# Kernel tuning notes

Measured on AMD Instinct MI355X. Metric: run time of the kernel, lower is better.

The kernel has to match this reference:

```python
import jax, jax.numpy as jnp
import numpy as np

DIM = 1024
MLP_RATIO = 4
EPS = 1e-6


def rmsnorm(x, w):
    return x * jax.lax.rsqrt(jnp.mean(x * x, axis=-1, keepdims=True) + EPS) * w


def film(x, cond, w, b):
    # cond: [B, D] -> scale/shift: [B, D] each, broadcast over tokens
    ss = cond @ w + b  # [B, 2D]
    scale, shift = jnp.split(ss, 2, axis=-1)
    return x * (1.0 + scale[:, None, :]) + shift[:, None, :]


def setup_inputs() -> dict:
    key = jax.random.key(0)
    ks = jax.random.split(key, 16)
    B, N, D = 4, 2048, DIM
    H = D * MLP_RATIO
    s = lambda fan_in: 1.0 / np.sqrt(fan_in)
    return {
        "x": jax.random.normal(ks[0], (B, N, D), jnp.float32),
        "cond": jax.random.normal(ks[1], (B, D), jnp.float32),
        "norm1_w": jnp.ones((D,), jnp.float32),
        "film1_w": jax.random.normal(ks[2], (D, 2 * D), jnp.float32) * s(D),
        "film1_b": jnp.zeros((2 * D,), jnp.float32),
        "q_w": jax.random.normal(ks[3], (D, D), jnp.float32) * s(D),
        "q_b": jnp.zeros((D,), jnp.float32),
        "k_w": jax.random.normal(ks[4], (D, D), jnp.float32) * s(D),
        "k_b": jnp.zeros((D,), jnp.float32),
        "v_w": jax.random.normal(ks[5], (D, D), jnp.float32) * s(D),
        "v_b": jnp.zeros((D,), jnp.float32),
        "proj_w": jax.random.normal(ks[6], (D, D), jnp.float32) * s(D),
        "proj_b": jnp.zeros((D,), jnp.float32),
        "norm2_w": jnp.ones((D,), jnp.float32),
        "film2_w": jax.random.normal(ks[7], (D, 2 * D), jnp.float32) * s(D),
        "film2_b": jnp.zeros((2 * D,), jnp.float32),
        "mlp_w1": jax.random.normal(ks[8], (D, H), jnp.float32) * s(D),
        "mlp_b1": jnp.zeros((H,), jnp.float32),
        "mlp_w2": jax.random.normal(ks[9], (H, D), jnp.float32) * s(H),
        "mlp_b2": jnp.zeros((D,), jnp.float32),
    }


def reference(x, cond, norm1_w, film1_w, film1_b, q_w, q_b, k_w, k_b, v_w, v_b,
              proj_w, proj_b, norm2_w, film2_w, film2_b, mlp_w1, mlp_b1,
              mlp_w2, mlp_b2):
    B, N, D = x.shape
    x_in = x
    h = film(rmsnorm(x, norm1_w), cond, film1_w, film1_b)
    Q = h @ q_w + q_b
    K = h @ k_w + k_b
    V = h @ v_w + v_b
    scores = jnp.einsum('bnd,bmd->bnm', Q, K) * (D ** -0.5)  # [B,N,N]
    attn = jax.nn.softmax(scores, axis=-1)
    out = jnp.einsum('bnm,bmd->bnd', attn, V)
    x = x_in + (out @ proj_w + proj_b)
    x_in = x
    h = film(rmsnorm(x, norm2_w), cond, film2_w, film2_b)
    h = jax.nn.gelu(h @ mlp_w1 + mlp_b1, approximate=False) @ mlp_w2 + mlp_b2
    return x_in + h
```

## Files before the change

kernel.cpp:

```cpp
#include <hip/hip_runtime.h>
#include <math.h>

typedef unsigned short u16;
typedef __bf16 bf16;
typedef bf16 bf16x8 __attribute__((ext_vector_type(8)));
typedef float f32x4 __attribute__((ext_vector_type(4)));

#define DEV __device__ __forceinline__
#define MFMA(a, b, c) __builtin_amdgcn_mfma_f32_16x16x32_bf16(a, b, c, 0, 0, 0)

DEV u16 f2b(float f) {
  unsigned u = __builtin_bit_cast(unsigned, f);
  u += 0x7fffu + ((u >> 16) & 1u);
  return (u16)(u >> 16);
}
DEV float b2f(u16 h) {
  unsigned u = ((unsigned)h) << 16;
  return __builtin_bit_cast(float, u);
}
DEV float gelu_f(float x) {
  float e = __expf(x * (-1.5957691216f - 0.07135481283f * x * x));
  return x / (1.0f + e);
}

DEV void gl2lds16(const void* g, void* l) {
  __builtin_amdgcn_global_load_lds(
      (const __attribute__((address_space(1))) unsigned int*)g,
      (__attribute__((address_space(3))) unsigned int*)l, 16, 0, 0);
}

struct TDesc { const float* src; u16* dst; int R, C, t0, tx; };
struct T6 { TDesc d[6]; };

__global__ void k_transpose6(T6 td) {
  __shared__ float tile[32][33];
  const int id = blockIdx.x;
  TDesc d = td.d[0];
#pragma unroll
  for (int k = 1; k < 6; ++k)
    if (id >= td.d[k].t0) d = td.d[k];
  const int local = id - d.t0;
  const int c0 = (local % d.tx) * 32, r0 = (local / d.tx) * 32;
  const int tx = threadIdx.x, ty = threadIdx.y;
#pragma unroll
  for (int i = 0; i < 32; i += 8)
    tile[ty + i][tx] = d.src[(long)(r0 + ty + i) * d.C + c0 + tx];
  __syncthreads();
#pragma unroll
  for (int i = 0; i < 32; i += 8)
    d.dst[(long)(c0 + ty + i) * d.R + r0 + tx] = f2b(tile[tx][ty + i]);
}

__global__ __launch_bounds__(256) void k_film_part(const float* __restrict__ cond,
                                                   const float* __restrict__ f1w,
                                                   const float* __restrict__ f2w,
                                                   float* __restrict__ part) {
  const int j = blockIdx.x * 256 + threadIdx.x;
  const int b = blockIdx.y;
  const int z = blockIdx.z;
  const int kz = z & 7;
  const float* fw = (z < 8) ? f1w : f2w;
  const float* cp = cond + b * 1024 + kz * 128;
  const float* wp = fw + (long)kz * 128 * 2048 + j;
  float acc = 0.0f;
#pragma unroll 4
  for (int d = 0; d < 128; ++d) acc = fmaf(cp[d], wp[(long)d * 2048], acc);
  part[((z * 4 + b) << 11) + j] = acc;
}
__global__ __launch_bounds__(256) void k_film_comb(const float* __restrict__ part,
                                                   const float* __restrict__ f1b,
                                                   const float* __restrict__ f2b_,
                                                   float* __restrict__ ss) {
  const int j = blockIdx.x * 256 + threadIdx.x;
  const int b = blockIdx.y & 3, f = blockIdx.y >> 2;
  float a = (f ? f2b_ : f1b)[j];
#pragma unroll
  for (int kz = 0; kz < 8; ++kz) a += part[(((f * 8 + kz) * 4 + b) << 11) + j];
  ss[((f * 4 + b) << 11) + j] = a;
}

template <typename InT>
__global__ __launch_bounds__(256) void k_rmsfilm(const InT* __restrict__ x,
                                                 const float* __restrict__ nw,
                                                 const float* __restrict__ ss,
                                                 u16* __restrict__ h) {
  const int row = blockIdx.x;
  const int b = row >> 11;
  const int t = threadIdx.x;
  float4 v;
  if constexpr (sizeof(InT) == 4) {
    v = ((const float4*)(x + (long)row * 1024))[t];
  } else {
    ushort4 u = ((const ushort4*)(x + (long)row * 1024))[t];
    v = make_float4(b2f(u.x), b2f(u.y), b2f(u.z), b2f(u.w));
  }
  float s = v.x * v.x + v.y * v.y + v.z * v.z + v.w * v.w;
#pragma unroll
  for (int off = 32; off; off >>= 1) s += __shfl_xor(s, off);
  __shared__ float red[4];
  const int wv = t >> 6, lane = t & 63;
  if (lane == 0) red[wv] = s;
  __syncthreads();
  const float tot = red[0] + red[1] + red[2] + red[3];
  const float rn = rsqrtf(tot * (1.0f / 1024.0f) + 1e-6f);
  const float4 w4 = ((const float4*)nw)[t];
  const float4 sc = ((const float4*)(ss + b * 2048))[t];
  const float4 sh = ((const float4*)(ss + b * 2048 + 1024))[t];
  ushort4 o;
  o.x = f2b(v.x * rn * w4.x * (1.0f + sc.x) + sh.x);
  o.y = f2b(v.y * rn * w4.y * (1.0f + sc.y) + sh.y);
  o.z = f2b(v.z * rn * w4.z * (1.0f + sc.z) + sh.z);
  o.w = f2b(v.w * rn * w4.w * (1.0f + sc.w) + sh.w);
  ((ushort4*)(h + (long)row * 1024))[t] = o;
}

__global__ __launch_bounds__(256) void k_rowsuminv(const float* __restrict__ part,
                                                   float* __restrict__ inv) {
  const int id = blockIdx.x * 256 + threadIdx.x;
  float s = 0.0f;
#pragma unroll
  for (int b = 0; b < 16; ++b) s += part[b * 8192 + id];
  inv[id] = 1.0f / s;
}

enum { EB = 1, ES = 2, EG = 4, ER = 8, EQKV = 16, ERB = 32, EEXP = 64, EPVN = 128 };

template <int BN, int EPI, typename OutT>
__global__ __launch_bounds__(256, 4) void k_gemm(
    const u16* __restrict__ A, const u16* __restrict__ B, OutT* __restrict__ C,
    const float* __restrict__ bias, const float* __restrict__ bias2,
    const float* __restrict__ bias3, const float* __restrict__ resid,
    u16* __restrict__ Vt, float* __restrict__ rsum, float scale,
    int N, int K, long sAb, long sBb, long sCb) {
  constexpr int NR = BN / 32;
  constexpr int NBC = BN * 8 / 256;
  __shared__ u16 As[128 * 64];
  __shared__ u16 Bs[BN * 64];
  const int tid = threadIdx.x, lane = tid & 63, wv = tid >> 6;
  const int wr = wv >> 1, wc = wv & 1;
  const int r = lane & 15, q = lane >> 4;

  int flat = blockIdx.y * gridDim.x + blockIdx.x;
  const int nxy = gridDim.x * gridDim.y;
  flat = (flat & 7) * (nxy >> 3) + (flat >> 3);
  const int bx = flat % gridDim.x, by = flat / gridDim.x;

  const long bm = (long)by * 128, bn = (long)bx * BN;
  const u16* Ab = A + (long)blockIdx.z * sAb + bm * K;
  const u16* Bb = B + (long)blockIdx.z * sBb + bn * K;

  f32x4 acc[4][NR] = {};

  for (int k0 = 0; k0 < K; k0 += 64) {
#pragma unroll
    for (int i = 0; i < 4; ++i) {
      const int c = i * 256 + tid;
      const int row = c >> 3, sp = c & 7;
      const long g = (long)row * K + k0 + ((sp ^ (row & 7)) << 3);
      gl2lds16(Ab + g, As + c * 8);
    }
#pragma unroll
    for (int i = 0; i < NBC; ++i) {
      const int c = i * 256 + tid;
      const int row = c >> 3, sp = c & 7;
      const long g = (long)row * K + k0 + ((sp ^ (row & 7)) << 3);
      gl2lds16(Bb + g, Bs + c * 8);
    }
    __syncthreads();
    bf16x8 a[8], b[2 * NR];
#pragma unroll
    for (int kh = 0; kh < 2; ++kh) {
#pragma unroll
      for (int i = 0; i < 4; ++i) {
        const int ar = wr * 64 + i * 16 + r;
        a[kh * 4 + i] = *(const bf16x8*)&As[ar * 64 + ((kh * 4 + q) ^ (ar & 7)) * 8];
      }
#pragma unroll
      for (int ni = 0; ni < NR; ++ni) {
        const int br = wc * (BN / 2) + ni * 16 + r;
        b[kh * NR + ni] = *(const bf16x8*)&Bs[br * 64 + ((kh * 4 + q) ^ (br & 7)) * 8];
      }
    }
#pragma unroll
    for (int kh = 0; kh < 2; ++kh)
#pragma unroll
      for (int mi = 0; mi < 4; ++mi)
#pragma unroll
        for (int ni = 0; ni < NR; ++ni)
          acc[mi][ni] = MFMA(a[kh * 4 + mi], b[kh * NR + ni], acc[mi][ni]);
    __syncthreads();
  }

  const long cb = (long)blockIdx.z * sCb;
  float rs[4][4] = {};
#pragma unroll
  for (int ni = 0; ni < NR; ++ni) {
    const long col = bn + wc * (BN / 2) + ni * 16 + r;
    float bv = 0.0f;
    int reg = 0, c = (int)col;
    if constexpr ((EPI & EB) != 0) bv = bias[col];
    if constexpr ((EPI & EQKV) != 0) {
      reg = (int)(col >> 10);
      c = (int)col & 1023;
      bv = (reg == 0) ? bias[c] : (reg == 1) ? bias2[c] : bias3[c];
    }
#pragma unroll
    for (int mi = 0; mi < 4; ++mi) {
#pragma unroll
      for (int j = 0; j < 4; ++j) {
        const long row = bm + wr * 64 + mi * 16 + q * 4 + j;
        float v = acc[mi][ni][j];
        if constexpr ((EPI & ES) != 0) v *= scale;
        if constexpr ((EPI & EEXP) != 0) {
          v = __expf(v * scale);
          rs[mi][j] += v;
        }
        if constexpr ((EPI & EPVN) != 0) v *= bias[(long)blockIdx.z * 2048 + row];
        if constexpr ((EPI & (EB | EQKV)) != 0) v += bv;
        if constexpr ((EPI & EG) != 0) v = gelu_f(v);
        if constexpr ((EPI & ER) != 0) v += resid[row * N + col];
        if constexpr ((EPI & ERB) != 0) v += b2f(((const u16*)resid)[row * N + col]);
        if constexpr ((EPI & EQKV) != 0) {
          if (reg < 2)
            ((u16*)C)[(long)reg * 8388608 + row * 1024 + c] = f2b(v);
          else
            Vt[((row >> 11) << 21) + ((long)c << 11) + (row & 2047)] = f2b(v);
        } else if constexpr (sizeof(OutT) == 4) {
          C[cb + row * N + col] = v;
        } else {
          C[cb + row * N + col] = f2b(v);
        }
      }
    }
  }
  if constexpr ((EPI & EEXP) != 0) {
    float* rbuf = (float*)As;
#pragma unroll
    for (int mi = 0; mi < 4; ++mi)
#pragma unroll
      for (int j = 0; j < 4; ++j) {
        float v = rs[mi][j];
        v += __shfl_xor(v, 1);
        v += __shfl_xor(v, 2);
        v += __shfl_xor(v, 4);
        v += __shfl_xor(v, 8);
        rs[mi][j] = v;
      }
    if (r == 0) {
#pragma unroll
      for (int mi = 0; mi < 4; ++mi)
#pragma unroll
        for (int j = 0; j < 4; ++j)
          rbuf[wc * 128 + wr * 64 + mi * 16 + q * 4 + j] = rs[mi][j];
    }
    __syncthreads();
    if (tid < 128) {
      const float s = rbuf[tid] + rbuf[128 + tid];
      rsum[(long)bx * 8192 + (long)blockIdx.z * 2048 + bm + tid] = s;
    }
  }
}

extern "C" void kernel_launch(void* const* d_in, const int* in_sizes, int n_in,
                              void* d_out, int out_size, void* d_ws, size_t ws_size,
                              hipStream_t stream) {
  const float* x    = (const float*)d_in[0];
  const float* cond = (const float*)d_in[1];
  const float* n1w  = (const float*)d_in[2];
  const float* f1w  = (const float*)d_in[3];
  const float* f1b  = (const float*)d_in[4];
  const float* qw   = (const float*)d_in[5];
  const float* qb   = (const float*)d_in[6];
  const float* kw   = (const float*)d_in[7];
  const float* kb   = (const float*)d_in[8];
  const float* vw   = (const float*)d_in[9];
  const float* vb   = (const float*)d_in[10];
  const float* pw   = (const float*)d_in[11];
  const float* pb   = (const float*)d_in[12];
  const float* n2w  = (const float*)d_in[13];
  const float* f2w  = (const float*)d_in[14];
  const float* f2b_ = (const float*)d_in[15];
  const float* w1   = (const float*)d_in[16];
  const float* b1   = (const float*)d_in[17];
  const float* w2   = (const float*)d_in[18];
  const float* b2   = (const float*)d_in[19];
  float* out = (float*)d_out;

  char* ws = (char*)d_ws;
  size_t o = 0;
  auto alloc = [&](size_t bytes) {
    size_t ret = o;
    o += (bytes + 255) & ~(size_t)255;
    return ret;
  };
  const long N = 2048, D = 1024, H = 4096;

  u16* qkvT = (u16*)(ws + alloc(3 * D * D * 2));
  u16* pT   = (u16*)(ws + alloc(D * D * 2));
  u16* w1T  = (u16*)(ws + alloc(D * H * 2));
  u16* w2T  = (u16*)(ws + alloc(D * H * 2));
  float* ss    = (float*)(ws + alloc(2 * 4 * 2 * D * 4));
  float* part  = (float*)(ws + alloc(16 * 4 * 2 * D * 4));
  float* spart = (float*)(ws + alloc(16 * 8192 * 4));
  float* rsinv = (float*)(ws + alloc(8192 * 4));
  u16* h    = (u16*)(ws + alloc(4 * N * D * 2));
  u16* x1b  = (u16*)(ws + alloc(4 * N * D * 2));
  u16* AO   = (u16*)(ws + alloc(4 * N * D * 2));
  const size_t big = o;
  u16* Q    = (u16*)(ws + alloc(4 * N * D * 2));
  u16* Kb   = (u16*)(ws + alloc(4 * N * D * 2));
  u16* Vt   = (u16*)(ws + alloc(4 * N * D * 2));
  u16* S    = (u16*)(ws + alloc(4 * N * N * 2));
  u16* h1   = (u16*)(ws + big);
  (void)ws_size; (void)in_sizes; (void)n_in; (void)out_size; (void)Kb;

  T6 td;
  td.d[0] = {qw, qkvT,                1024, 1024,    0,  32};
  td.d[1] = {kw, qkvT + 1024 * 1024,  1024, 1024, 1024,  32};
  td.d[2] = {vw, qkvT + 2048 * 1024,  1024, 1024, 2048,  32};
  td.d[3] = {pw, pT,                  1024, 1024, 3072,  32};
  td.d[4] = {w1, w1T,                 1024, 4096, 4096, 128};
  td.d[5] = {w2, w2T,                 4096, 1024, 8192,  32};
  k_transpose6<<<12288, dim3(32, 8), 0, stream>>>(td);

  k_film_part<<<dim3(8, 4, 16), 256, 0, stream>>>(cond, f1w, f2w, part);
  k_film_comb<<<dim3(8, 8), 256, 0, stream>>>(part, f1b, f2b_, ss);

  k_rmsfilm<float><<<8192, 256, 0, stream>>>(x, n1w, ss, h);

  k_gemm<128, EQKV, u16><<<dim3(24, 64, 1), 256, 0, stream>>>(
      h, qkvT, Q, qb, kb, vb, nullptr, Vt, nullptr, 1.0f, 3072, 1024, 0, 0, 0);

  k_gemm<128, EEXP, u16><<<dim3(16, 16, 4), 256, 0, stream>>>(
      Q, Kb, S, nullptr, nullptr, nullptr, nullptr, nullptr, spart, 0.03125f,
      2048, 1024, N * D, N * D, N * N);
  k_rowsuminv<<<32, 256, 0, stream>>>(spart, rsinv);

  k_gemm<64, EPVN, u16><<<dim3(16, 16, 4), 256, 0, stream>>>(
      S, Vt, AO, rsinv, nullptr, nullptr, nullptr, nullptr, nullptr, 1.0f,
      1024, 2048, N * N, D * N, N * D);

  k_gemm<64, EB | ER, u16><<<dim3(16, 64, 1), 256, 0, stream>>>(
      AO, pT, x1b, pb, nullptr, nullptr, x, nullptr, nullptr, 1.0f, 1024, 1024, 0, 0, 0);

  k_rmsfilm<u16><<<8192, 256, 0, stream>>>(x1b, n2w, ss + 4 * 2048, h);

  k_gemm<128, EB | EG, u16><<<dim3(32, 64, 1), 256, 0, stream>>>(
      h, w1T, h1, b1, nullptr, nullptr, nullptr, nullptr, nullptr, 1.0f, 4096, 1024, 0, 0, 0);

  k_gemm<64, EB | ERB, float><<<dim3(16, 64, 1), 256, 0, stream>>>(
      h1, w2T, out, b2, nullptr, nullptr, (const float*)x1b, nullptr, nullptr, 1.0f,
      1024, 4096, 0, 0, 0);
}
```

Measured before the change: 394.1 us.

## Add 256x256 double-buffered 8-wave GEMM kernel for QKV, QK^T and MLP1

```diff
diff --git a/kernel.cpp b/kernel.cpp
--- a/kernel.cpp
+++ b/kernel.cpp
@@ -8,6 +8,7 @@
 
 #define DEV __device__ __forceinline__
 #define MFMA(a, b, c) __builtin_amdgcn_mfma_f32_16x16x32_bf16(a, b, c, 0, 0, 0)
+#define FENCE() asm volatile("" ::: "memory")
 
 DEV u16 f2b(float f) {
   unsigned u = __builtin_bit_cast(unsigned, f);
@@ -119,11 +120,186 @@
   const int id = blockIdx.x * 256 + threadIdx.x;
   float s = 0.0f;
 #pragma unroll
-  for (int b = 0; b < 16; ++b) s += part[b * 8192 + id];
+  for (int b = 0; b < 8; ++b) s += part[b * 8192 + id];
   inv[id] = 1.0f / s;
 }
 
 enum { EB = 1, ES = 2, EG = 4, ER = 8, EQKV = 16, ERB = 32, EEXP = 64, EPVN = 128 };
+
+template <int EPI, typename OutT>
+__global__ __launch_bounds__(512, 2) void k_gemm8(
+    const u16* __restrict__ A, const u16* __restrict__ B, OutT* __restrict__ C,
+    const float* __restrict__ bias, const float* __restrict__ bias2,
+    const float* __restrict__ bias3, u16* __restrict__ Vt,
+    float* __restrict__ rsum, float scale, int N, int K,
+    long sAb, long sBb, long sCb) {
+  __shared__ u16 sm[65536];
+  const int tid = threadIdx.x, lane = tid & 63, wid = tid >> 6;
+  const int wm = wid >> 2, wn = wid & 3;
+  const int r = lane & 15, q = lane >> 4;
+
+  int flat = blockIdx.y * gridDim.x + blockIdx.x;
+  const int nxy = gridDim.x * gridDim.y;
+  flat = (flat & 7) * (nxy >> 3) + (flat >> 3);
+  const int bx = flat % gridDim.x, by = flat / gridDim.x;
+
+  const long bm = (long)by * 256, bn = (long)bx * 256;
+  const u16* Ab = A + (long)blockIdx.z * sAb + bm * K;
+  const u16* Bb = B + (long)blockIdx.z * sBb + bn * K;
+  const int NT = K >> 6;
+
+#define STG(buf, ab, half, t)                                                   \
+  {                                                                             \
+    const u16* _s = (ab) ? Bb : Ab;                                             \
+    u16* _d = &sm[(buf) * 32768 + (ab) * 16384 + (half) * 8192];                \
+    _Pragma("unroll") for (int _i = 0; _i < 2; ++_i) {                          \
+      const int _c = _i * 512 + tid;                                            \
+      const int _row = _c >> 3, _sp = _c & 7;                                   \
+      gl2lds16(_s + (long)((half) * 128 + _row) * K + (long)(t) * 64 +          \
+                   ((_sp ^ (_row & 7)) << 3),                                   \
+               _d + _c * 8);                                                    \
+    }                                                                           \
+  }
+#define LDAq(dst, buf, qm)                                                      \
+  _Pragma("unroll") for (int _p = 0; _p < 4; ++_p)                              \
+  _Pragma("unroll") for (int _kk = 0; _kk < 2; ++_kk) {                         \
+    const int _ar = wm * 128 + (qm) * 64 + _p * 16 + r;                         \
+    dst[_p * 2 + _kk] = *(const bf16x8*)&sm[(buf) * 32768 +                     \
+        (_ar >> 7) * 8192 + (_ar & 127) * 64 + (((_kk * 4 + q) ^ (_ar & 7)) << 3)]; \
+  }
+#define LDBq(dst, buf, qn)                                                      \
+  _Pragma("unroll") for (int _p = 0; _p < 2; ++_p)                              \
+  _Pragma("unroll") for (int _kk = 0; _kk < 2; ++_kk) {                         \
+    const int _br = wn * 64 + (qn) * 32 + _p * 16 + r;                          \
+    dst[_p * 2 + _kk] = *(const bf16x8*)&sm[(buf) * 32768 + 16384 +             \
+        (_br >> 7) * 8192 + (_br & 127) * 64 + (((_kk * 4 + q) ^ (_br & 7)) << 3)]; \
+  }
+#define BAR() { FENCE(); __builtin_amdgcn_s_barrier(); FENCE(); }
+#define WAITMM() { asm volatile("s_waitcnt lgkmcnt(0)" ::: "memory"); \
+                   __builtin_amdgcn_sched_barrier(0); }
+#define VMW4() asm volatile("s_waitcnt vmcnt(4)" ::: "memory")
+#define VMW0() asm volatile("s_waitcnt vmcnt(0)" ::: "memory")
+#define MM(aa, bb, qm, qn)                                                      \
+  { __builtin_amdgcn_s_setprio(1);                                              \
+    _Pragma("unroll") for (int _p = 0; _p < 4; ++_p)                            \
+    _Pragma("unroll") for (int _n = 0; _n < 2; ++_n)                            \
+    _Pragma("unroll") for (int _kk = 0; _kk < 2; ++_kk)                         \
+      acc[(qm) * 4 + _p][(qn) * 2 + _n] =                                       \
+          MFMA(aa[_p * 2 + _kk], bb[_n * 2 + _kk], acc[(qm) * 4 + _p][(qn) * 2 + _n]); \
+    __builtin_amdgcn_s_setprio(0); }
+
+  f32x4 acc[8][4] = {};
+  STG(0, 1, 0, 0); STG(0, 1, 1, 0); STG(0, 0, 0, 0); STG(0, 0, 1, 0);
+  STG(1, 1, 0, 1); STG(1, 1, 1, 1);
+  VMW4();
+  BAR();
+
+  for (int i = 0; i < (NT >> 1); ++i) {
+    const int T = 2 * i;
+    const bool more = (T + 2) < NT;
+    bf16x8 a[8], b0[4], b1[4];
+    LDAq(a, 0, 0); LDBq(b0, 0, 0);
+    STG(1, 0, 0, T + 1);
+    BAR(); WAITMM(); MM(a, b0, 0, 0); BAR();
+    LDBq(b1, 0, 1);
+    STG(1, 0, 1, T + 1);
+    BAR(); WAITMM(); MM(a, b1, 0, 1); BAR();
+    LDAq(a, 0, 1);
+    if (more) STG(0, 1, 0, T + 2);
+    BAR(); WAITMM(); MM(a, b1, 1, 1); BAR();
+    if (more) { STG(0, 1, 1, T + 2); VMW4(); }
+    else VMW0();
+    BAR(); WAITMM(); MM(a, b0, 1, 0); BAR();
+    LDAq(a, 1, 0); LDBq(b0, 1, 0);
+    if (more) STG(0, 0, 0, T + 2);
+    BAR(); WAITMM(); MM(a, b0, 0, 0); BAR();
+    LDBq(b1, 1, 1);
+    if (more) STG(0, 0, 1, T + 2);
+    BAR(); WAITMM(); MM(a, b1, 0, 1); BAR();
+    LDAq(a, 1, 1);
+    if (more) STG(1, 1, 0, T + 3);
+    BAR(); WAITMM(); MM(a, b1, 1, 1); BAR();
+    if (more) { STG(1, 1, 1, T + 3); VMW4(); }
+    else VMW0();
+    BAR(); WAITMM(); MM(a, b0, 1, 0); BAR();
+  }
+
+  const long cb = (long)blockIdx.z * sCb;
+  float rs[8][4];
+  if constexpr ((EPI & EEXP) != 0) {
+#pragma unroll
+    for (int mi = 0; mi < 8; ++mi)
+#pragma unroll
+      for (int j = 0; j < 4; ++j) rs[mi][j] = 0.0f;
+  }
+#pragma unroll
+  for (int ni = 0; ni < 4; ++ni) {
+    const long col = bn + wn * 64 + ni * 16 + r;
+    float bv = 0.0f;
+    int reg = 0, c = (int)col;
+    if constexpr ((EPI & EB) != 0) bv = bias[col];
+    if constexpr ((EPI & EQKV) != 0) {
+      reg = (int)(col >> 10);
+      c = (int)col & 1023;
+      bv = (reg == 0) ? bias[c] : (reg == 1) ? bias2[c] : bias3[c];
+    }
+#pragma unroll
+    for (int mi = 0; mi < 8; ++mi) {
+#pragma unroll
+      for (int j = 0; j < 4; ++j) {
+        const long row = bm + wm * 128 + mi * 16 + q * 4 + j;
+        float v = acc[mi][ni][j];
+        if constexpr ((EPI & EEXP) != 0) { v = __expf(v * scale); rs[mi][j] += v; }
+        if constexpr ((EPI & (EB | EQKV)) != 0) v += bv;
+        if constexpr ((EPI & EG) != 0) v = gelu_f(v);
+        if constexpr ((EPI & EQKV) != 0) {
+          if (reg < 2)
+            ((u16*)C)[(long)reg * 8388608 + row * 1024 + c] = f2b(v);
+          else
+            Vt[((row >> 11) << 21) + ((long)c << 11) + (row & 2047)] = f2b(v);
+        } else if constexpr (sizeof(OutT) == 4) {
+          C[cb + row * N + col] = v;
+        } else {
+          C[cb + row * N + col] = f2b(v);
+        }
+      }
+    }
+  }
+  if constexpr ((EPI & EEXP) != 0) {
+    float* rbuf = (float*)sm;
+    __syncthreads();
+#pragma unroll
+    for (int mi = 0; mi < 8; ++mi)
+#pragma unroll
+      for (int j = 0; j < 4; ++j) {
+        float v = rs[mi][j];
+        v += __shfl_xor(v, 1);
+        v += __shfl_xor(v, 2);
+        v += __shfl_xor(v, 4);
+        v += __shfl_xor(v, 8);
+        rs[mi][j] = v;
+      }
+    if (r == 0) {
+#pragma unroll
+      for (int mi = 0; mi < 8; ++mi)
+#pragma unroll
+        for (int j = 0; j < 4; ++j)
+          rbuf[wn * 256 + wm * 128 + mi * 16 + q * 4 + j] = rs[mi][j];
+    }
+    __syncthreads();
+    if (tid < 256)
+      rsum[(long)bx * 8192 + (long)blockIdx.z * 2048 + bm + tid] =
+          rbuf[tid] + rbuf[256 + tid] + rbuf[512 + tid] + rbuf[768 + tid];
+  }
+#undef STG
+#undef LDAq
+#undef LDBq
+#undef BAR
+#undef WAITMM
+#undef VMW4
+#undef VMW0
+#undef MM
+}
 
 template <int BN, int EPI, typename OutT>
 __global__ __launch_bounds__(256, 4) void k_gemm(
@@ -144,6 +320,7 @@
   const int nxy = gridDim.x * gridDim.y;
   flat = (flat & 7) * (nxy >> 3) + (flat >> 3);
   const int bx = flat % gridDim.x, by = flat / gridDim.x;
+  (void)bx;
 
   const long bm = (long)by * 128, bn = (long)bx * BN;
   const u16* Ab = A + (long)blockIdx.z * sAb + bm * K;
@@ -192,18 +369,11 @@
   }
 
   const long cb = (long)blockIdx.z * sCb;
-  float rs[4][4] = {};
 #pragma unroll
   for (int ni = 0; ni < NR; ++ni) {
     const long col = bn + wc * (BN / 2) + ni * 16 + r;
     float bv = 0.0f;
-    int reg = 0, c = (int)col;
     if constexpr ((EPI & EB) != 0) bv = bias[col];
-    if constexpr ((EPI & EQKV) != 0) {
-      reg = (int)(col >> 10);
-      c = (int)col & 1023;
-      bv = (reg == 0) ? bias[c] : (reg == 1) ? bias2[c] : bias3[c];
-    }
 #pragma unroll
     for (int mi = 0; mi < 4; ++mi) {
 #pragma unroll
@@ -211,21 +381,12 @@
         const long row = bm + wr * 64 + mi * 16 + q * 4 + j;
         float v = acc[mi][ni][j];
         if constexpr ((EPI & ES) != 0) v *= scale;
-        if constexpr ((EPI & EEXP) != 0) {
-          v = __expf(v * scale);
-          rs[mi][j] += v;
-        }
         if constexpr ((EPI & EPVN) != 0) v *= bias[(long)blockIdx.z * 2048 + row];
-        if constexpr ((EPI & (EB | EQKV)) != 0) v += bv;
+        if constexpr ((EPI & EB) != 0) v += bv;
         if constexpr ((EPI & EG) != 0) v = gelu_f(v);
         if constexpr ((EPI & ER) != 0) v += resid[row * N + col];
         if constexpr ((EPI & ERB) != 0) v += b2f(((const u16*)resid)[row * N + col]);
-        if constexpr ((EPI & EQKV) != 0) {
-          if (reg < 2)
-            ((u16*)C)[(long)reg * 8388608 + row * 1024 + c] = f2b(v);
-          else
-            Vt[((row >> 11) << 21) + ((long)c << 11) + (row & 2047)] = f2b(v);
-        } else if constexpr (sizeof(OutT) == 4) {
+        if constexpr (sizeof(OutT) == 4) {
           C[cb + row * N + col] = v;
         } else {
           C[cb + row * N + col] = f2b(v);
@@ -233,32 +394,7 @@
       }
     }
   }
-  if constexpr ((EPI & EEXP) != 0) {
-    float* rbuf = (float*)As;
-#pragma unroll
-    for (int mi = 0; mi < 4; ++mi)
-#pragma unroll
-      for (int j = 0; j < 4; ++j) {
-        float v = rs[mi][j];
-        v += __shfl_xor(v, 1);
-        v += __shfl_xor(v, 2);
-        v += __shfl_xor(v, 4);
-        v += __shfl_xor(v, 8);
-        rs[mi][j] = v;
-      }
-    if (r == 0) {
-#pragma unroll
-      for (int mi = 0; mi < 4; ++mi)
-#pragma unroll
-        for (int j = 0; j < 4; ++j)
-          rbuf[wc * 128 + wr * 64 + mi * 16 + q * 4 + j] = rs[mi][j];
-    }
-    __syncthreads();
-    if (tid < 128) {
-      const float s = rbuf[tid] + rbuf[128 + tid];
-      rsum[(long)bx * 8192 + (long)blockIdx.z * 2048 + bm + tid] = s;
-    }
-  }
+  (void)Vt; (void)rsum; (void)bias2; (void)bias3;
 }
 
 extern "C" void kernel_launch(void* const* d_in, const int* in_sizes, int n_in,
@@ -328,11 +464,11 @@
 
   k_rmsfilm<float><<<8192, 256, 0, stream>>>(x, n1w, ss, h);
 
-  k_gemm<128, EQKV, u16><<<dim3(24, 64, 1), 256, 0, stream>>>(
-      h, qkvT, Q, qb, kb, vb, nullptr, Vt, nullptr, 1.0f, 3072, 1024, 0, 0, 0);
-
-  k_gemm<128, EEXP, u16><<<dim3(16, 16, 4), 256, 0, stream>>>(
-      Q, Kb, S, nullptr, nullptr, nullptr, nullptr, nullptr, spart, 0.03125f,
+  k_gemm8<EQKV, u16><<<dim3(12, 32, 1), 512, 0, stream>>>(
+      h, qkvT, Q, qb, kb, vb, Vt, nullptr, 1.0f, 3072, 1024, 0, 0, 0);
+
+  k_gemm8<EEXP, u16><<<dim3(8, 8, 4), 512, 0, stream>>>(
+      Q, Kb, S, nullptr, nullptr, nullptr, nullptr, spart, 0.03125f,
       2048, 1024, N * D, N * D, N * N);
   k_rowsuminv<<<32, 256, 0, stream>>>(spart, rsinv);
 
@@ -345,8 +481,8 @@
 
   k_rmsfilm<u16><<<8192, 256, 0, stream>>>(x1b, n2w, ss + 4 * 2048, h);
 
-  k_gemm<128, EB | EG, u16><<<dim3(32, 64, 1), 256, 0, stream>>>(
-      h, w1T, h1, b1, nullptr, nullptr, nullptr, nullptr, nullptr, 1.0f, 4096, 1024, 0, 0, 0);
+  k_gemm8<EB | EG, u16><<<dim3(16, 32, 1), 512, 0, stream>>>(
+      h, w1T, h1, b1, nullptr, nullptr, nullptr, nullptr, 1.0f, 4096, 1024, 0, 0, 0);
 
   k_gemm<64, EB | ERB, float><<<dim3(16, 64, 1), 256, 0, stream>>>(
       h1, w2T, out, b2, nullptr, nullptr, (const float*)x1b, nullptr, nullptr, 1.0f,
```

After: 453.7 us. 1.15x slower.

## Stage GEMM epilogue through LDS for vectorized coalesced stores

Applied to the files above, without the earlier changes.

```diff
diff --git a/kernel.cpp b/kernel.cpp
--- a/kernel.cpp
+++ b/kernel.cpp
@@ -2,6 +2,7 @@
 #include <math.h>
 
 typedef unsigned short u16;
+typedef unsigned int u32;
 typedef __bf16 bf16;
 typedef bf16 bf16x8 __attribute__((ext_vector_type(8)));
 typedef float f32x4 __attribute__((ext_vector_type(4)));
@@ -192,47 +193,115 @@
   }
 
   const long cb = (long)blockIdx.z * sCb;
-  float rs[4][4] = {};
+  constexpr bool VMODE = ((EPI & EQKV) != 0);
+  const bool isV = VMODE && (bx >= 16);
+  float rs[4][4];
+  if constexpr ((EPI & EEXP) != 0) {
+#pragma unroll
+    for (int mi = 0; mi < 4; ++mi)
+#pragma unroll
+      for (int j = 0; j < 4; ++j) rs[mi][j] = 0.0f;
+  }
+  float* lb = (float*)As;
+
 #pragma unroll
   for (int ni = 0; ni < NR; ++ni) {
     const long col = bn + wc * (BN / 2) + ni * 16 + r;
     float bv = 0.0f;
-    int reg = 0, c = (int)col;
     if constexpr ((EPI & EB) != 0) bv = bias[col];
-    if constexpr ((EPI & EQKV) != 0) {
-      reg = (int)(col >> 10);
-      c = (int)col & 1023;
-      bv = (reg == 0) ? bias[c] : (reg == 1) ? bias2[c] : bias3[c];
-    }
+    if constexpr (VMODE) {
+      const int c = (int)col & 1023;
+      bv = (bx < 8) ? bias[c] : (bx < 16) ? bias2[c] : bias3[c];
+    }
+    ushort4 vo[4];
 #pragma unroll
     for (int mi = 0; mi < 4; ++mi) {
+      float vj[4];
 #pragma unroll
       for (int j = 0; j < 4; ++j) {
-        const long row = bm + wr * 64 + mi * 16 + q * 4 + j;
         float v = acc[mi][ni][j];
         if constexpr ((EPI & ES) != 0) v *= scale;
         if constexpr ((EPI & EEXP) != 0) {
           v = __expf(v * scale);
           rs[mi][j] += v;
         }
-        if constexpr ((EPI & EPVN) != 0) v *= bias[(long)blockIdx.z * 2048 + row];
-        if constexpr ((EPI & (EB | EQKV)) != 0) v += bv;
+        if constexpr ((EPI & EPVN) != 0) {
+          const long row = bm + wr * 64 + mi * 16 + q * 4 + j;
+          v *= bias[(long)blockIdx.z * 2048 + row];
+        }
+        v += bv;
         if constexpr ((EPI & EG) != 0) v = gelu_f(v);
-        if constexpr ((EPI & ER) != 0) v += resid[row * N + col];
-        if constexpr ((EPI & ERB) != 0) v += b2f(((const u16*)resid)[row * N + col]);
-        if constexpr ((EPI & EQKV) != 0) {
-          if (reg < 2)
-            ((u16*)C)[(long)reg * 8388608 + row * 1024 + c] = f2b(v);
-          else
-            Vt[((row >> 11) << 21) + ((long)c << 11) + (row & 2047)] = f2b(v);
+        vj[j] = v;
+      }
+      if constexpr (VMODE) {
+        vo[mi].x = f2b(vj[0]); vo[mi].y = f2b(vj[1]);
+        vo[mi].z = f2b(vj[2]); vo[mi].w = f2b(vj[3]);
+      }
+      if (!isV) {
+#pragma unroll
+        for (int j = 0; j < 4; ++j)
+          lb[(wr * 64 + mi * 16 + q * 4 + j) * 32 + wc * 16 + r] = vj[j];
+      }
+    }
+    if constexpr (VMODE) {
+      if (isV) {
+        const int c = (int)col & 1023;
+#pragma unroll
+        for (int mi = 0; mi < 4; ++mi) {
+          const long row = bm + wr * 64 + mi * 16 + q * 4;
+          *(ushort4*)&Vt[((row >> 11) << 21) + ((long)c << 11) + (row & 2047)] = vo[mi];
+        }
+      }
+    }
+    __syncthreads();
+    if (!isV) {
+#pragma unroll
+      for (int s = 0; s < 2; ++s) {
+        const int ch = s * 256 + tid;
+        const int row128 = ch >> 2, cc = ch & 3;
+        const long grow = bm + row128;
+        const long gcol = bn + (long)(cc >> 1) * (BN / 2) + ni * 16 + (cc & 1) * 8;
+        float v8[8];
+#pragma unroll
+        for (int k = 0; k < 8; ++k) v8[k] = lb[row128 * 32 + cc * 8 + k];
+        if constexpr ((EPI & ER) != 0) {
+          const float4 r0 = *(const float4*)&resid[grow * N + gcol];
+          const float4 r1 = *(const float4*)&resid[grow * N + gcol + 4];
+          v8[0] += r0.x; v8[1] += r0.y; v8[2] += r0.z; v8[3] += r0.w;
+          v8[4] += r1.x; v8[5] += r1.y; v8[6] += r1.z; v8[7] += r1.w;
+        }
+        if constexpr ((EPI & ERB) != 0) {
+          const ushort4 r0 = *(const ushort4*)&((const u16*)resid)[grow * N + gcol];
+          const ushort4 r1 = *(const ushort4*)&((const u16*)resid)[grow * N + gcol + 4];
+          v8[0] += b2f(r0.x); v8[1] += b2f(r0.y); v8[2] += b2f(r0.z); v8[3] += b2f(r0.w);
+          v8[4] += b2f(r1.x); v8[5] += b2f(r1.y); v8[6] += b2f(r1.z); v8[7] += b2f(r1.w);
+        }
+        if constexpr (VMODE) {
+          u16* dst = (u16*)C + ((bx < 8) ? 0L : 8388608L);
+          uint4 o;
+          o.x = (u32)f2b(v8[0]) | ((u32)f2b(v8[1]) << 16);
+          o.y = (u32)f2b(v8[2]) | ((u32)f2b(v8[3]) << 16);
+          o.z = (u32)f2b(v8[4]) | ((u32)f2b(v8[5]) << 16);
+          o.w = (u32)f2b(v8[6]) | ((u32)f2b(v8[7]) << 16);
+          *(uint4*)&dst[grow * 1024 + (gcol & 1023)] = o;
         } else if constexpr (sizeof(OutT) == 4) {
-          C[cb + row * N + col] = v;
+          float4 f0 = {v8[0], v8[1], v8[2], v8[3]};
+          float4 f1 = {v8[4], v8[5], v8[6], v8[7]};
+          *(float4*)&C[cb + grow * N + gcol] = f0;
+          *(float4*)&C[cb + grow * N + gcol + 4] = f1;
         } else {
-          C[cb + row * N + col] = f2b(v);
-        }
-      }
-    }
+          uint4 o;
+          o.x = (u32)f2b(v8[0]) | ((u32)f2b(v8[1]) << 16);
+          o.y = (u32)f2b(v8[2]) | ((u32)f2b(v8[3]) << 16);
+          o.z = (u32)f2b(v8[4]) | ((u32)f2b(v8[5]) << 16);
+          o.w = (u32)f2b(v8[6]) | ((u32)f2b(v8[7]) << 16);
+          *(uint4*)&((u16*)C)[cb + grow * N + gcol] = o;
+        }
+      }
+    }
+    __syncthreads();
   }
+
   if constexpr ((EPI & EEXP) != 0) {
     float* rbuf = (float*)As;
 #pragma unroll
@@ -246,6 +315,7 @@
         v += __shfl_xor(v, 8);
         rs[mi][j] = v;
       }
+    __syncthreads();
     if (r == 0) {
 #pragma unroll
       for (int mi = 0; mi < 4; ++mi)
@@ -259,6 +329,7 @@
       rsum[(long)bx * 8192 + (long)blockIdx.z * 2048 + bm + tid] = s;
     }
   }
+  (void)Vt; (void)rsum; (void)bias2; (void)bias3; (void)resid;
 }
 
 extern "C" void kernel_launch(void* const* d_in, const int* in_sizes, int n_in,
```

Measured after the change: 393.0 us. No clear change (-0.3%).
